# Kernel tuning notes

Measured on AMD Instinct MI355X. Metric: run time of the kernel, lower is better.

## Reference

```python
import jax, jax.numpy as jnp
import numpy as np

B, S, D, H = 4, 2048, 1024, 16
HD = D // H
ROPE_THETA = 10000.0


def setup_inputs() -> dict:
    key = jax.random.key(0)
    ks = jax.random.split(key, 5)
    scale = 1.0 / np.sqrt(D)
    inp = {
        "x": jax.random.normal(ks[0], (B, S, D), dtype=jnp.float32),
        "Wq": jax.random.normal(ks[1], (D, D), dtype=jnp.float32) * scale,
        "bq": jnp.zeros((D,), jnp.float32),
        "Wk": jax.random.normal(ks[2], (D, D), dtype=jnp.float32) * scale,
        "bk": jnp.zeros((D,), jnp.float32),
        "Wv": jax.random.normal(ks[3], (D, D), dtype=jnp.float32) * scale,
        "bv": jnp.zeros((D,), jnp.float32),
        "Wo": jax.random.normal(ks[4], (D, D), dtype=jnp.float32) * scale,
        "bo": jnp.zeros((D,), jnp.float32),
        # causal mask: True means masked (j > i), matching masked_fill semantics
        "attn_mask": jnp.triu(jnp.ones((S, S), dtype=bool), k=1),
    }
    return inp


def _rope(x):
    # x: [B, H, S, HD]; half-split rotary embedding
    half = HD // 2
    inv_freq = 1.0 / (ROPE_THETA ** (jnp.arange(0, half, dtype=jnp.float32) / half))
    pos = jnp.arange(x.shape[2], dtype=jnp.float32)
    freqs = pos[:, None] * inv_freq[None, :]            # [S, half]
    cos = jnp.cos(freqs)[None, None]                    # [1,1,S,half]
    sin = jnp.sin(freqs)[None, None]
    x1, x2 = x[..., :half], x[..., half:]
    return jnp.concatenate([x1 * cos - x2 * sin, x2 * cos + x1 * sin], axis=-1)


def reference(x, Wq, bq, Wk, bk, Wv, bv, Wo, bo, attn_mask):
    def shape(t):  # [B,S,D] -> [B,H,S,HD]
        return t.reshape(B, S, H, HD).transpose(0, 2, 1, 3)

    q = shape(x @ Wq.T + bq)
    k = shape(x @ Wk.T + bk)
    v = shape(x @ Wv.T + bv)
    q = _rope(q)
    k = _rope(k)
    scores = jnp.einsum("bhqd,bhkd->bhqk", q, k) * (HD ** -0.5)
    scores = jnp.where(attn_mask[None, None], -jnp.inf, scores)
    w = jax.nn.softmax(scores, axis=-1)
    attn = jnp.einsum("bhqk,bhkd->bhqd", w, v)
    merged = attn.transpose(0, 2, 1, 3).reshape(B, S, D)
    return merged @ Wo.T + bo
```

## Files before the change

kernel.cpp:

```cpp
#include <hip/hip_runtime.h>
#include <math.h>

#define BATCH 4
#define SEQ   2048
#define DMODEL 1024
#define NHEAD 16
#define HDIM  64
#define MROWS (BATCH*SEQ)

typedef unsigned short u16;
typedef unsigned int   u32;

using bf16x8 = __attribute__((ext_vector_type(8))) short;
using f32x4  = __attribute__((ext_vector_type(4))) float;
using f32x16 = __attribute__((ext_vector_type(16))) float;
using u32x4  = __attribute__((ext_vector_type(4))) unsigned int;

__device__ __forceinline__ u16 f2bf(float f) {
    u32 u = __float_as_uint(f);
    u += 0x7fffu + ((u >> 16) & 1u);
    return (u16)(u >> 16);
}
__device__ __forceinline__ u32 pack2bf(float a, float b) {
    u32 ua = __float_as_uint(a); ua += 0x7fffu + ((ua >> 16) & 1u);
    u32 ub = __float_as_uint(b); ub += 0x7fffu + ((ub >> 16) & 1u);
    return (ua >> 16) | (ub & 0xffff0000u);
}
__device__ __forceinline__ u32 cvtpk(float a, float b) {
    u32 r;
    asm("v_cvt_pk_bf16_f32 %0, %1, %2" : "=v"(r) : "v"(a), "v"(b));
    return r;
}
#define PLSWAP(a, b) asm("v_permlane32_swap_b32 %0, %1" : "+v"(a), "+v"(b))

#define GLOBAL_LOAD_LDS16(gp, lp)                                              \
    __builtin_amdgcn_global_load_lds(                                          \
        (const __attribute__((address_space(1))) void*)(gp),                   \
        (__attribute__((address_space(3))) void*)(lp), 16, 0, 0)

__global__ __launch_bounds__(256) void convert_inputs(
    const float* __restrict__ x,  const float* __restrict__ wq,
    const float* __restrict__ wk, const float* __restrict__ wv,
    const float* __restrict__ wo, u16* __restrict__ dst)
{
    long long i4 = ((long long)blockIdx.x * 256 + threadIdx.x) * 4;
    const float* src; long long off;
    if (i4 < 8388608LL) { src = x; off = i4; }
    else {
        long long j = i4 - 8388608LL;
        int seg = (int)(j >> 20);
        off = j & 1048575LL;
        src = (seg == 0) ? wq : (seg == 1) ? wk : (seg == 2) ? wv : wo;
    }
    float4 v = *(const float4*)(src + off);
    u32 lo = (u32)f2bf(v.x) | ((u32)f2bf(v.y) << 16);
    u32 hi = (u32)f2bf(v.z) | ((u32)f2bf(v.w) << 16);
    *(uint2*)(dst + i4) = make_uint2(lo, hi);
}

template<int QKV>
__global__ __launch_bounds__(512) void gemm_mfma(
    const u16* __restrict__ A,
    const u16* __restrict__ Wq_, const u16* __restrict__ Wk_, const u16* __restrict__ Wv_,
    const float* __restrict__ bq_, const float* __restrict__ bk_, const float* __restrict__ bv_,
    u16* __restrict__ Cq_, u16* __restrict__ Ck_, u16* __restrict__ Cv_,
    float* __restrict__ Cf)
{
    __shared__ u16 As[3 * 256 * 64];
    __shared__ u16 Ws[3 * 128 * 64];

    const int t    = threadIdx.x;
    const int lane = t & 63;
    const int w    = t >> 6;
    const int quad = lane >> 4;
    const int l15  = lane & 15;
    const int wm   = w >> 1;
    const int wn   = w & 1;

    const int bx  = blockIdx.x;
    const int xcd = bx & 7;
    const int i_  = bx >> 3;
    const int bml = i_ & 3;
    const int n_  = i_ >> 2;
    const int seg = (QKV ? (n_ >> 3) : 0);
    const int nn  = (QKV ? (n_ & 7) : n_);

    const u16*   W    = (seg == 0) ? Wq_ : (seg == 1) ? Wk_ : Wv_;
    const float* bias = (seg == 0) ? bq_ : (seg == 1) ? bk_ : bv_;
    u16*         Cb   = (seg == 0) ? Cq_ : (seg == 1) ? Ck_ : Cv_;

    const int bm   = (xcd * 4 + bml) * 256;
    const int bn   = nn * 128;
    const int wrow = wm * 64;
    const int wcol = wn * 64;

    const int sr8 = lane >> 3;
    const int scl = (lane & 7) ^ sr8;
    const u16* gA = A + (size_t)(bm + 8 * w + sr8) * DMODEL + scl * 8;
    const u16* gB = W + (size_t)(bn + 8 * w + sr8) * DMODEL + scl * 8;

#define STAGE_A(li, kt, bs)                                                    \
    GLOBAL_LOAD_LDS16(gA + (size_t)(li) * 64 * DMODEL + (kt) * 64,             \
                      &As[(bs) * 16384 + ((li) * 64 + 8 * w) * 64])
#define STAGE_B(li, kt, bs)                                                    \
    GLOBAL_LOAD_LDS16(gB + (size_t)(li) * 64 * DMODEL + (kt) * 64,             \
                      &Ws[(bs) * 8192 + ((li) * 64 + 8 * w) * 64])

    STAGE_A(0, 0, 0); STAGE_A(1, 0, 0); STAGE_A(2, 0, 0); STAGE_A(3, 0, 0);
    STAGE_B(0, 0, 0); STAGE_B(1, 0, 0);
    STAGE_A(0, 1, 1); STAGE_A(1, 1, 1); STAGE_A(2, 1, 1); STAGE_A(3, 1, 1);
    STAGE_B(0, 1, 1); STAGE_B(1, 1, 1);
    asm volatile("s_waitcnt vmcnt(6)" ::: "memory");
    __builtin_amdgcn_s_barrier();

    const int c0 = (quad ^ (l15 & 7)) * 8;
    const int c1 = c0 ^ 32;

    f32x4 acc[4][4] = {};

    int bsel = 0;
    for (int kt = 0; kt < DMODEL / 64; ++kt) {
        const u16* Ab = &As[bsel * 16384];
        const u16* Bb = &Ws[bsel * 8192];
        const int  ks = kt + 2;
        const int  sb = (bsel >= 1) ? bsel - 1 : 2;
        const bool st = (ks < DMODEL / 64);

        bf16x8 af[4], bf[4];

        #pragma unroll
        for (int i = 0; i < 4; ++i)
            af[i] = *(const bf16x8*)&Ab[(wrow + 16 * i + l15) * 64 + c0];
        #pragma unroll
        for (int j = 0; j < 4; ++j)
            bf[j] = *(const bf16x8*)&Bb[(wcol + 16 * j + l15) * 64 + c0];
        if (st) { STAGE_A(0, ks, sb); STAGE_A(1, ks, sb); STAGE_A(2, ks, sb); }
        __builtin_amdgcn_s_barrier();
        __builtin_amdgcn_s_setprio(1);
        #pragma unroll
        for (int i = 0; i < 4; ++i)
            #pragma unroll
            for (int j = 0; j < 4; ++j)
                acc[i][j] = __builtin_amdgcn_mfma_f32_16x16x32_bf16(af[i], bf[j], acc[i][j], 0, 0, 0);
        __builtin_amdgcn_s_setprio(0);
        __builtin_amdgcn_s_barrier();

        #pragma unroll
        for (int i = 0; i < 4; ++i)
            af[i] = *(const bf16x8*)&Ab[(wrow + 16 * i + l15) * 64 + c1];
        #pragma unroll
        for (int j = 0; j < 4; ++j)
            bf[j] = *(const bf16x8*)&Bb[(wcol + 16 * j + l15) * 64 + c1];
        if (st) { STAGE_A(3, ks, sb); STAGE_B(0, ks, sb); STAGE_B(1, ks, sb); }
        __builtin_amdgcn_s_barrier();
        __builtin_amdgcn_s_setprio(1);
        #pragma unroll
        for (int i = 0; i < 4; ++i)
            #pragma unroll
            for (int j = 0; j < 4; ++j)
                acc[i][j] = __builtin_amdgcn_mfma_f32_16x16x32_bf16(af[i], bf[j], acc[i][j], 0, 0, 0);
        __builtin_amdgcn_s_setprio(0);
        if (st) asm volatile("s_waitcnt vmcnt(6)" ::: "memory");
        else    asm volatile("s_waitcnt vmcnt(0)" ::: "memory");
        __builtin_amdgcn_s_barrier();

        bsel = (bsel == 2) ? 0 : bsel + 1;
    }
#undef STAGE_A
#undef STAGE_B

    float bv[4];
    #pragma unroll
    for (int j = 0; j < 4; j++) bv[j] = bias[bn + wcol + 16 * j + l15];

    if constexpr (QKV == 0) {
        #pragma unroll
        for (int i = 0; i < 4; i++)
            #pragma unroll
            for (int r = 0; r < 4; r++) {
                int mg = bm + wrow + 16 * i + quad * 4 + r;
                #pragma unroll
                for (int j = 0; j < 4; j++)
                    Cf[(size_t)mg * DMODEL + bn + wcol + 16 * j + l15] = acc[i][j][r] + bv[j];
            }
    } else {
        if (seg == 2) {
            u16* T = As;
            #pragma unroll
            for (int i = 0; i < 4; i++) {
                #pragma unroll
                for (int j = 0; j < 4; j++) {
                    int col = wrow + 16 * i + quad * 4;
                    int row = wcol + 16 * j + l15;
                    u32 lo = pack2bf(acc[i][j][0] + bv[j], acc[i][j][1] + bv[j]);
                    u32 hi = pack2bf(acc[i][j][2] + bv[j], acc[i][j][3] + bv[j]);
                    *(uint2*)((char*)T + row * 512 + ((col * 2) ^ ((row & 3) << 4)))
                        = make_uint2(lo, hi);
                }
            }
            __syncthreads();
            {
                int row  = t >> 2, colc = t & 3;
                int hgl  = (bn + row) >> 6;
                int dl   = (bn + row) & 63;
                int bb   = bm >> 11;
                size_t obase = (((size_t)(bb * NHEAD + hgl)) * HDIM + dl) * SEQ
                             + (bm & (SEQ - 1)) + colc * 64;
                #pragma unroll
                for (int k = 0; k < 8; k++) {
                    uint4 vv = *(const uint4*)((const char*)T + row * 512
                                 + ((colc * 128 + k * 16) ^ ((row & 3) << 4)));
                    *(uint4*)(Cb + obase + k * 8) = vv;
                }
            }
        } else {
            const float qscale = (seg == 0) ? 0.18033688011112042f : 1.0f;
            float inv[2];
            #pragma unroll
            for (int j = 0; j < 2; j++) {
                int d = 16 * j + l15;
                inv[j] = exp2f(-(float)d * 0.4152410118609203f);
            }
            #pragma unroll
            for (int i = 0; i < 4; i++)
                #pragma unroll
                for (int r = 0; r < 4; r++) {
                    int mg = bm + wrow + 16 * i + quad * 4 + r;
                    int s  = mg & (SEQ - 1);
                    #pragma unroll
                    for (int j = 0; j < 2; j++) {
                        float f = (float)s * inv[j];
                        float sn, cs;
                        __sincosf(f, &sn, &cs);
                        float a1 = acc[i][j][r]     + bv[j];
                        float a2 = acc[i][j + 2][r] + bv[j + 2];
                        float o1 = (a1 * cs - a2 * sn) * qscale;
                        float o2 = (a2 * cs + a1 * sn) * qscale;
                        Cb[(size_t)mg * DMODEL + bn + wcol + 16 * j       + l15] = f2bf(o1);
                        Cb[(size_t)mg * DMODEL + bn + wcol + 16 * (j + 2) + l15] = f2bf(o2);
                    }
                }
        }
    }
}

__global__ __launch_bounds__(256) void attn_mfma(
    const u16* __restrict__ Q, const u16* __restrict__ K,
    const u16* __restrict__ VT, u16* __restrict__ O)
{
    __shared__ __align__(16) u16 smem[16640];
    u16* const Qs  = smem;
    u16* const Ks0 = smem + 8192;
    u16* const Ks1 = smem;
    u16* const Vt0 = smem + 12288;
    u16* const Vt1 = smem + 4096;
    float* const lS = (float*)(smem + 16384);

    const int t    = threadIdx.x;
    const int lane = t & 63;
    const int w    = t >> 6;
    const int l31  = lane & 31;
    const int hl   = lane >> 5;
    const int bid  = blockIdx.x;
    const int bh   = bid & 63;
    const int x_   = bid >> 6, g_ = x_ >> 2, r_ = x_ & 3;
    const int qt   = (g_ == 0) ? 15 - r_ : (g_ == 1) ? 8 + r_
                   : (g_ == 2) ? 4 + r_ : 3 - r_;
    const int h    = bh & (NHEAD - 1);
    const int b    = bh >> 4;
    const int q0   = qt * 128;

    const size_t gbase = ((size_t)b * SEQ) * DMODEL + h * HDIM;
    const size_t vbase = ((size_t)(b * NHEAD + h)) * HDIM * SEQ;

    const int rl  = lane >> 3;
    const int csw = (lane & 7) ^ rl;

    #pragma unroll
    for (int i = 0; i < 4; i++) {
        int row = 32 * w + 8 * i + rl;
        GLOBAL_LOAD_LDS16(Q + gbase + (size_t)(q0 + row) * DMODEL + csw * 8,
                          &Qs[(32 * w + 8 * i) * 64]);
    }
    #pragma unroll
    for (int i = 0; i < 2; i++) {
        int row = 16 * w + 8 * i + rl;
        GLOBAL_LOAD_LDS16(K + gbase + (size_t)row * DMODEL + csw * 8,
                          &Ks0[(16 * w + 8 * i) * 64]);
        GLOBAL_LOAD_LDS16(VT + vbase + (size_t)row * SEQ + csw * 8,
                          &Vt0[(16 * w + 8 * i) * 64]);
    }
    __syncthreads();

    bf16x8 qf[4];
    {
        int row = 32 * w + l31;
        #pragma unroll
        for (int s = 0; s < 4; s++) {
            int c = (hl + 2 * s) ^ (row & 7);
            qf[s] = *(const bf16x8*)&Qs[row * 64 + c * 8];
        }
    }
    __syncthreads();

    float lsum = 0.0f;
    f32x16 oacc[2] = {};
    const int qg   = q0 + 32 * w + l31;
    const int qmax = q0 + 32 * w + 31;

#define QUADRANT(KRH, F0, F1) do {                                             \
    f32x16 s_ = {};                                                            \
    __builtin_amdgcn_s_setprio(1);                                             \
    _Pragma("unroll")                                                          \
    for (int stp_ = 0; stp_ < 4; ++stp_) {                                     \
        int c_ = ((hl + 2 * stp_) ^ (l31 & 7)) * 8;                            \
        bf16x8 ka_ = *(const bf16x8*)&Ksb[(32 * (KRH) + l31) * 64 + c_];       \
        s_ = __builtin_amdgcn_mfma_f32_32x32x16_bf16(ka_, qf[stp_], s_, 0, 0, 0);\
    }                                                                          \
    __builtin_amdgcn_s_setprio(0);                                             \
    if (k0 + 32 * (KRH) + 31 > q0 + 32 * w) {                                  \
        _Pragma("unroll")                                                      \
        for (int rr_ = 0; rr_ < 16; ++rr_) {                                   \
            int krg_ = k0 + 32 * (KRH) + (rr_ & 3) + 8 * (rr_ >> 2) + 4 * hl;  \
            if (krg_ > qg) s_[rr_] = -1e30f;                                   \
        }                                                                      \
    }                                                                          \
    float pv_[16];                                                             \
    _Pragma("unroll")                                                          \
    for (int rr_ = 0; rr_ < 16; ++rr_) pv_[rr_] = __builtin_amdgcn_exp2f(s_[rr_]);\
    lsum += ((pv_[0]+pv_[1])+(pv_[2]+pv_[3])) + ((pv_[4]+pv_[5])+(pv_[6]+pv_[7]))\
          + ((pv_[8]+pv_[9])+(pv_[10]+pv_[11])) + ((pv_[12]+pv_[13])+(pv_[14]+pv_[15]));\
    u32 k01_ = cvtpk(pv_[0], pv_[1]),   k23_ = cvtpk(pv_[2], pv_[3]);          \
    u32 k45_ = cvtpk(pv_[4], pv_[5]),   k67_ = cvtpk(pv_[6], pv_[7]);          \
    u32 k89_ = cvtpk(pv_[8], pv_[9]),   kab_ = cvtpk(pv_[10], pv_[11]);        \
    u32 kcd_ = cvtpk(pv_[12], pv_[13]), kef_ = cvtpk(pv_[14], pv_[15]);        \
    PLSWAP(k01_, k45_); PLSWAP(k23_, k67_);                                    \
    PLSWAP(k89_, kcd_); PLSWAP(kab_, kef_);                                    \
    { union { u32x4 u; bf16x8 v; } c0_; c0_.u = (u32x4){k01_, k23_, k45_, k67_};\
      F0 = c0_.v; }                                                            \
    { union { u32x4 u; bf16x8 v; } c1_; c1_.u = (u32x4){k89_, kab_, kcd_, kef_};\
      F1 = c1_.v; }                                                            \
} while (0)

#define PVSTEP(STP, PF) do {                                                   \
    int c_ = ((hl + 2 * (STP)) ^ (l31 & 7)) * 8;                               \
    bf16x8 v0_ = *(const bf16x8*)&Vtb[l31 * 64 + c_];                          \
    bf16x8 v1_ = *(const bf16x8*)&Vtb[(32 + l31) * 64 + c_];                   \
    oacc[0] = __builtin_amdgcn_mfma_f32_32x32x16_bf16(PF, v0_, oacc[0], 0, 0, 0);\
    oacc[1] = __builtin_amdgcn_mfma_f32_32x32x16_bf16(PF, v1_, oacc[1], 0, 0, 0);\
} while (0)

    const int ktn = 2 * qt + 2;
    for (int kt = 0; kt < ktn; kt++) {
        const int k0 = kt * 64;
        u16* const Ksb = (kt & 1) ? Ks1 : Ks0;
        u16* const Vtb = (kt & 1) ? Vt1 : Vt0;

        if (kt + 1 < ktn) {
            u16* const Ksn = (kt & 1) ? Ks0 : Ks1;
            u16* const Vtn = (kt & 1) ? Vt0 : Vt1;
            const size_t kk0 = (size_t)(kt + 1) * 64;
            #pragma unroll
            for (int i = 0; i < 2; i++) {
                int row = 16 * w + 8 * i + rl;
                GLOBAL_LOAD_LDS16(K + gbase + (kk0 + row) * DMODEL + csw * 8,
                                  &Ksn[(16 * w + 8 * i) * 64]);
                GLOBAL_LOAD_LDS16(VT + vbase + (size_t)row * SEQ + kk0 + csw * 8,
                                  &Vtn[(16 * w + 8 * i) * 64]);
            }
        }

        if (k0 <= qmax) {
            const bool q2 = (k0 + 32 <= qmax);
            bf16x8 pa0, pa1, pa2, pa3;
            QUADRANT(0, pa0, pa1);
            __builtin_amdgcn_s_setprio(1);
            PVSTEP(0, pa0); PVSTEP(1, pa1);
            __builtin_amdgcn_s_setprio(0);
            if (q2) {
                QUADRANT(1, pa2, pa3);
                __builtin_amdgcn_s_setprio(1);
                PVSTEP(2, pa2); PVSTEP(3, pa3);
                __builtin_amdgcn_s_setprio(0);
            }
        }
        asm volatile("s_waitcnt vmcnt(0)" ::: "memory");
        __builtin_amdgcn_s_barrier();
    }
#undef QUADRANT
#undef PVSTEP

    lsum += __shfl_xor(lsum, 32, 64);
    if (lane < 32) lS[32 * w + lane] = lsum;
    __syncthreads();

    #pragma unroll
    for (int g = 0; g < 4; g++) {
        f32x4 lv = *(const f32x4*)&lS[32 * w + 8 * g + 4 * hl];
        #pragma unroll
        for (int rr = 0; rr < 4; rr++) {
            int qg2 = q0 + 32 * w + rr + 8 * g + 4 * hl;
            float inv = 1.0f / lv[rr];
            #pragma unroll
            for (int dh = 0; dh < 2; dh++) {
                float o = oacc[dh][4 * g + rr] * inv;
                O[gbase + (size_t)qg2 * DMODEL + 32 * dh + l31] = f2bf(o);
            }
        }
    }
}

extern "C" void kernel_launch(void* const* d_in, const int* in_sizes, int n_in,
                              void* d_out, int out_size, void* d_ws, size_t ws_size,
                              hipStream_t stream)
{
    const float* x  = (const float*)d_in[0];
    const float* Wq = (const float*)d_in[1];
    const float* bq = (const float*)d_in[2];
    const float* Wk = (const float*)d_in[3];
    const float* bk = (const float*)d_in[4];
    const float* Wv = (const float*)d_in[5];
    const float* bv = (const float*)d_in[6];
    const float* Wo = (const float*)d_in[7];
    const float* bo = (const float*)d_in[8];

    u16* wsp = (u16*)d_ws;
    u16* xb  = wsp;
    u16* Wqb = wsp + 8388608;
    u16* Wkb = Wqb + 1048576;
    u16* Wvb = Wkb + 1048576;
    u16* Wob = Wvb + 1048576;
    u16* Qb  = Wob + 1048576;
    u16* Kb  = Qb + 8388608;
    u16* Vb  = Kb + 8388608;
    u16* Ab  = Vb + 8388608;

    convert_inputs<<<12288, 256, 0, stream>>>(x, Wq, Wk, Wv, Wo, xb);

    gemm_mfma<1><<<768, 512, 0, stream>>>(xb, Wqb, Wkb, Wvb, bq, bk, bv,
                                          Qb, Kb, Vb, nullptr);

    attn_mfma<<<1024, 256, 0, stream>>>(Qb, Kb, Vb, Ab);

    gemm_mfma<0><<<256, 512, 0, stream>>>(Ab, Wob, nullptr, nullptr, bo, nullptr, nullptr,
                                          nullptr, nullptr, nullptr, (float*)d_out);
}
```

Before: 254.6 us.

## Enlarge GEMM tile to 256x256 with double-buffered 8-phase pipelined K loop

The QKV and output-projection GEMMs move from 256x128 block tiles with a triple-buffered LDS pipeline to 256x256 tiles. Each wave now computes 128x64, with B fragments kept in registers across four sub-phases and loads of the next K tile interleaved between phases. Grid sizes are halved to 384 and 128 blocks. The aim is more arithmetic intensity per LDS and global byte. The costs are more accumulator registers (128 fp32), fewer blocks than the GPU has CUs for the output projection, and a larger LDS swizzle for the V transpose.

```diff
diff --git a/kernel.cpp b/kernel.cpp
--- a/kernel.cpp
+++ b/kernel.cpp
@@ -66,150 +66,162 @@
     u16* __restrict__ Cq_, u16* __restrict__ Ck_, u16* __restrict__ Cv_,
     float* __restrict__ Cf)
 {
-    __shared__ u16 As[3 * 256 * 64];
-    __shared__ u16 Ws[3 * 128 * 64];
+    __shared__ __align__(16) u16 smem[65536];
 
     const int t    = threadIdx.x;
     const int lane = t & 63;
     const int w    = t >> 6;
     const int quad = lane >> 4;
     const int l15  = lane & 15;
-    const int wm   = w >> 1;
-    const int wn   = w & 1;
+    const int wm   = w >> 2;
+    const int wn   = w & 3;
 
     const int bx  = blockIdx.x;
     const int xcd = bx & 7;
     const int i_  = bx >> 3;
     const int bml = i_ & 3;
     const int n_  = i_ >> 2;
-    const int seg = (QKV ? (n_ >> 3) : 0);
-    const int nn  = (QKV ? (n_ & 7) : n_);
+    const int seg = (QKV ? (n_ >> 2) : 0);
+    const int nn  = (QKV ? (n_ & 3) : n_);
 
     const u16*   W    = (seg == 0) ? Wq_ : (seg == 1) ? Wk_ : Wv_;
     const float* bias = (seg == 0) ? bq_ : (seg == 1) ? bk_ : bv_;
     u16*         Cb   = (seg == 0) ? Cq_ : (seg == 1) ? Ck_ : Cv_;
 
-    const int bm   = (xcd * 4 + bml) * 256;
-    const int bn   = nn * 128;
-    const int wrow = wm * 64;
-    const int wcol = wn * 64;
+    const int bm = (xcd * 4 + bml) * 256;
+    const int bn = nn * 256;
 
     const int sr8 = lane >> 3;
     const int scl = (lane & 7) ^ sr8;
     const u16* gA = A + (size_t)(bm + 8 * w + sr8) * DMODEL + scl * 8;
     const u16* gB = W + (size_t)(bn + 8 * w + sr8) * DMODEL + scl * 8;
 
-#define STAGE_A(li, kt, bs)                                                    \
-    GLOBAL_LOAD_LDS16(gA + (size_t)(li) * 64 * DMODEL + (kt) * 64,             \
-                      &As[(bs) * 16384 + ((li) * 64 + 8 * w) * 64])
-#define STAGE_B(li, kt, bs)                                                    \
-    GLOBAL_LOAD_LDS16(gB + (size_t)(li) * 64 * DMODEL + (kt) * 64,             \
-                      &Ws[(bs) * 8192 + ((li) * 64 + 8 * w) * 64])
-
-    STAGE_A(0, 0, 0); STAGE_A(1, 0, 0); STAGE_A(2, 0, 0); STAGE_A(3, 0, 0);
-    STAGE_B(0, 0, 0); STAGE_B(1, 0, 0);
-    STAGE_A(0, 1, 1); STAGE_A(1, 1, 1); STAGE_A(2, 1, 1); STAGE_A(3, 1, 1);
-    STAGE_B(0, 1, 1); STAGE_B(1, 1, 1);
+#define STG_A(rg, kt, bs)                                                      \
+    GLOBAL_LOAD_LDS16(gA + (size_t)(rg) * 64 * DMODEL + (kt) * 64,             \
+                      &smem[(bs) * 16384 + ((rg) * 64 + 8 * w) * 64])
+#define STG_B(rg, kt, bs)                                                      \
+    GLOBAL_LOAD_LDS16(gB + (size_t)(rg) * 64 * DMODEL + (kt) * 64,             \
+                      &smem[32768 + (bs) * 16384 + ((rg) * 64 + 8 * w) * 64])
+
+    STG_B(0, 0, 0); STG_B(1, 0, 0); STG_B(2, 0, 0); STG_B(3, 0, 0);
+    STG_A(0, 0, 0); STG_A(2, 0, 0); STG_A(1, 0, 0); STG_A(3, 0, 0);
+    STG_B(0, 1, 1); STG_B(1, 1, 1); STG_B(2, 1, 1); STG_B(3, 1, 1);
+    STG_A(0, 1, 1); STG_A(2, 1, 1);
     asm volatile("s_waitcnt vmcnt(6)" ::: "memory");
     __builtin_amdgcn_s_barrier();
 
-    const int c0 = (quad ^ (l15 & 7)) * 8;
-    const int c1 = c0 ^ 32;
-
-    f32x4 acc[4][4] = {};
-
-    int bsel = 0;
-    for (int kt = 0; kt < DMODEL / 64; ++kt) {
-        const u16* Ab = &As[bsel * 16384];
-        const u16* Bb = &Ws[bsel * 8192];
-        const int  ks = kt + 2;
-        const int  sb = (bsel >= 1) ? bsel - 1 : 2;
-        const bool st = (ks < DMODEL / 64);
-
-        bf16x8 af[4], bf[4];
-
-        #pragma unroll
-        for (int i = 0; i < 4; ++i)
-            af[i] = *(const bf16x8*)&Ab[(wrow + 16 * i + l15) * 64 + c0];
-        #pragma unroll
-        for (int j = 0; j < 4; ++j)
-            bf[j] = *(const bf16x8*)&Bb[(wcol + 16 * j + l15) * 64 + c0];
-        if (st) { STAGE_A(0, ks, sb); STAGE_A(1, ks, sb); STAGE_A(2, ks, sb); }
-        __builtin_amdgcn_s_barrier();
-        __builtin_amdgcn_s_setprio(1);
-        #pragma unroll
-        for (int i = 0; i < 4; ++i)
-            #pragma unroll
-            for (int j = 0; j < 4; ++j)
-                acc[i][j] = __builtin_amdgcn_mfma_f32_16x16x32_bf16(af[i], bf[j], acc[i][j], 0, 0, 0);
-        __builtin_amdgcn_s_setprio(0);
-        __builtin_amdgcn_s_barrier();
-
-        #pragma unroll
-        for (int i = 0; i < 4; ++i)
-            af[i] = *(const bf16x8*)&Ab[(wrow + 16 * i + l15) * 64 + c1];
-        #pragma unroll
-        for (int j = 0; j < 4; ++j)
-            bf[j] = *(const bf16x8*)&Bb[(wcol + 16 * j + l15) * 64 + c1];
-        if (st) { STAGE_A(3, ks, sb); STAGE_B(0, ks, sb); STAGE_B(1, ks, sb); }
-        __builtin_amdgcn_s_barrier();
-        __builtin_amdgcn_s_setprio(1);
-        #pragma unroll
-        for (int i = 0; i < 4; ++i)
-            #pragma unroll
-            for (int j = 0; j < 4; ++j)
-                acc[i][j] = __builtin_amdgcn_mfma_f32_16x16x32_bf16(af[i], bf[j], acc[i][j], 0, 0, 0);
-        __builtin_amdgcn_s_setprio(0);
-        if (st) asm volatile("s_waitcnt vmcnt(6)" ::: "memory");
-        else    asm volatile("s_waitcnt vmcnt(0)" ::: "memory");
-        __builtin_amdgcn_s_barrier();
-
-        bsel = (bsel == 2) ? 0 : bsel + 1;
-    }
-#undef STAGE_A
-#undef STAGE_B
-
-    float bv[4];
+    const int cA0 = (quad ^ (l15 & 7)) * 8;
+
+    f32x4 acc[8][4] = {};
+    bf16x8 bfr[4][2];
+
+#define LOAD_B(Bb) {                                                           \
+    _Pragma("unroll")                                                          \
+    for (int j = 0; j < 4; ++j) {                                              \
+        bfr[j][0] = *(const bf16x8*)&(Bb)[(wn * 64 + 16 * j + l15) * 64 + cA0];\
+        bfr[j][1] = *(const bf16x8*)&(Bb)[(wn * 64 + 16 * j + l15) * 64 + (cA0 ^ 32)];\
+    } }
+#define PHASE(q, Ab, Bb, STAGES, CKPT) {                                       \
+    bf16x8 af_[2][2];                                                          \
+    if ((q) == 0) LOAD_B(Bb);                                                  \
+    _Pragma("unroll")                                                          \
+    for (int ii = 0; ii < 2; ++ii) {                                           \
+        const int r_ = (wm * 128 + (q) * 32 + 16 * ii + l15) * 64;             \
+        af_[ii][0] = *(const bf16x8*)&(Ab)[r_ + cA0];                          \
+        af_[ii][1] = *(const bf16x8*)&(Ab)[r_ + (cA0 ^ 32)];                   \
+    }                                                                          \
+    STAGES;                                                                    \
+    __builtin_amdgcn_s_barrier();                                              \
+    asm volatile("s_waitcnt lgkmcnt(0)" ::: "memory");                         \
+    __builtin_amdgcn_sched_barrier(0);                                         \
+    __builtin_amdgcn_s_setprio(1);                                             \
+    _Pragma("unroll")                                                          \
+    for (int ii = 0; ii < 2; ++ii)                                             \
+        _Pragma("unroll")                                                      \
+        for (int j = 0; j < 4; ++j) {                                          \
+            acc[2*(q)+ii][j] = __builtin_amdgcn_mfma_f32_16x16x32_bf16(        \
+                af_[ii][0], bfr[j][0], acc[2*(q)+ii][j], 0, 0, 0);             \
+            acc[2*(q)+ii][j] = __builtin_amdgcn_mfma_f32_16x16x32_bf16(        \
+                af_[ii][1], bfr[j][1], acc[2*(q)+ii][j], 0, 0, 0);             \
+        }                                                                      \
+    __builtin_amdgcn_s_setprio(0);                                             \
+    CKPT;                                                                      \
+    __builtin_amdgcn_s_barrier();                                              \
+}
+
+    #pragma unroll 1
+    for (int i = 0; i < 8; ++i) {
+        const bool st = (i < 7);
+        const int  kn = 2 * i + 2, kn3 = 2 * i + 3, ko = 2 * i + 1;
+        {
+            const u16* Ab = smem;
+            const u16* Bb = smem + 32768;
+            PHASE(0, Ab, Bb, { STG_A(1, ko, 1); STG_A(3, ko, 1); }, {});
+            PHASE(1, Ab, Bb, { if (st) { STG_B(0, kn, 0); STG_B(1, kn, 0); } }, {});
+            PHASE(2, Ab, Bb, { if (st) { STG_B(2, kn, 0); STG_B(3, kn, 0); } }, {});
+            PHASE(3, Ab, Bb, { if (st) { STG_A(0, kn, 0); STG_A(2, kn, 0); } },
+                  { if (st) asm volatile("s_waitcnt vmcnt(6)" ::: "memory");
+                    else    asm volatile("s_waitcnt vmcnt(0)" ::: "memory"); });
+        }
+        {
+            const u16* Ab = smem + 16384;
+            const u16* Bb = smem + 32768 + 16384;
+            PHASE(0, Ab, Bb, { if (st) { STG_A(1, kn, 0); STG_A(3, kn, 0); } }, {});
+            PHASE(1, Ab, Bb, { if (st) { STG_B(0, kn3, 1); STG_B(1, kn3, 1); } }, {});
+            PHASE(2, Ab, Bb, { if (st) { STG_B(2, kn3, 1); STG_B(3, kn3, 1); } }, {});
+            PHASE(3, Ab, Bb, { if (st) { STG_A(0, kn3, 1); STG_A(2, kn3, 1); } },
+                  { if (st) asm volatile("s_waitcnt vmcnt(6)" ::: "memory");
+                    else    asm volatile("s_waitcnt vmcnt(0)" ::: "memory"); });
+        }
+    }
+#undef PHASE
+#undef LOAD_B
+#undef STG_A
+#undef STG_B
+
+    const int wrow = wm * 128;
+    const int wcol = wn * 64;
+    float bvv[4];
     #pragma unroll
-    for (int j = 0; j < 4; j++) bv[j] = bias[bn + wcol + 16 * j + l15];
+    for (int j = 0; j < 4; j++) bvv[j] = bias[bn + wcol + 16 * j + l15];
 
     if constexpr (QKV == 0) {
         #pragma unroll
-        for (int i = 0; i < 4; i++)
+        for (int ri = 0; ri < 8; ri++)
             #pragma unroll
             for (int r = 0; r < 4; r++) {
-                int mg = bm + wrow + 16 * i + quad * 4 + r;
+                int mg = bm + wrow + 16 * ri + quad * 4 + r;
                 #pragma unroll
                 for (int j = 0; j < 4; j++)
-                    Cf[(size_t)mg * DMODEL + bn + wcol + 16 * j + l15] = acc[i][j][r] + bv[j];
+                    Cf[(size_t)mg * DMODEL + bn + wcol + 16 * j + l15] = acc[ri][j][r] + bvv[j];
             }
     } else {
         if (seg == 2) {
-            u16* T = As;
-            #pragma unroll
-            for (int i = 0; i < 4; i++) {
+            u16* T = smem;
+            #pragma unroll
+            for (int ri = 0; ri < 8; ri++) {
                 #pragma unroll
                 for (int j = 0; j < 4; j++) {
-                    int col = wrow + 16 * i + quad * 4;
+                    int col = wrow + 16 * ri + quad * 4;
                     int row = wcol + 16 * j + l15;
-                    u32 lo = pack2bf(acc[i][j][0] + bv[j], acc[i][j][1] + bv[j]);
-                    u32 hi = pack2bf(acc[i][j][2] + bv[j], acc[i][j][3] + bv[j]);
-                    *(uint2*)((char*)T + row * 512 + ((col * 2) ^ ((row & 3) << 4)))
+                    u32 lo = pack2bf(acc[ri][j][0] + bvv[j], acc[ri][j][1] + bvv[j]);
+                    u32 hi = pack2bf(acc[ri][j][2] + bvv[j], acc[ri][j][3] + bvv[j]);
+                    *(uint2*)((char*)T + row * 512 + ((col * 2) ^ ((row & 7) << 4)))
                         = make_uint2(lo, hi);
                 }
             }
             __syncthreads();
             {
-                int row  = t >> 2, colc = t & 3;
-                int hgl  = (bn + row) >> 6;
-                int dl   = (bn + row) & 63;
-                int bb   = bm >> 11;
+                int row = t >> 1, half = t & 1;
+                int hgl = (bn + row) >> 6;
+                int dl  = (bn + row) & 63;
+                int bb  = bm >> 11;
                 size_t obase = (((size_t)(bb * NHEAD + hgl)) * HDIM + dl) * SEQ
-                             + (bm & (SEQ - 1)) + colc * 64;
+                             + (bm & (SEQ - 1)) + half * 128;
                 #pragma unroll
-                for (int k = 0; k < 8; k++) {
+                for (int k = 0; k < 16; k++) {
                     uint4 vv = *(const uint4*)((const char*)T + row * 512
-                                 + ((colc * 128 + k * 16) ^ ((row & 3) << 4)));
+                                 + ((half * 256 + k * 16) ^ ((row & 7) << 4)));
                     *(uint4*)(Cb + obase + k * 8) = vv;
                 }
             }
@@ -222,18 +234,18 @@
                 inv[j] = exp2f(-(float)d * 0.4152410118609203f);
             }
             #pragma unroll
-            for (int i = 0; i < 4; i++)
+            for (int ri = 0; ri < 8; ri++)
                 #pragma unroll
                 for (int r = 0; r < 4; r++) {
-                    int mg = bm + wrow + 16 * i + quad * 4 + r;
+                    int mg = bm + wrow + 16 * ri + quad * 4 + r;
                     int s  = mg & (SEQ - 1);
                     #pragma unroll
                     for (int j = 0; j < 2; j++) {
                         float f = (float)s * inv[j];
                         float sn, cs;
                         __sincosf(f, &sn, &cs);
-                        float a1 = acc[i][j][r]     + bv[j];
-                        float a2 = acc[i][j + 2][r] + bv[j + 2];
+                        float a1 = acc[ri][j][r]     + bvv[j];
+                        float a2 = acc[ri][j + 2][r] + bvv[j + 2];
                         float o1 = (a1 * cs - a2 * sn) * qscale;
                         float o2 = (a2 * cs + a1 * sn) * qscale;
                         Cb[(size_t)mg * DMODEL + bn + wcol + 16 * j       + l15] = f2bf(o1);
@@ -437,11 +449,11 @@
 
     convert_inputs<<<12288, 256, 0, stream>>>(x, Wq, Wk, Wv, Wo, xb);
 
-    gemm_mfma<1><<<768, 512, 0, stream>>>(xb, Wqb, Wkb, Wvb, bq, bk, bv,
+    gemm_mfma<1><<<384, 512, 0, stream>>>(xb, Wqb, Wkb, Wvb, bq, bk, bv,
                                           Qb, Kb, Vb, nullptr);
 
     attn_mfma<<<1024, 256, 0, stream>>>(Qb, Kb, Vb, Ab);
 
-    gemm_mfma<0><<<256, 512, 0, stream>>>(Ab, Wob, nullptr, nullptr, bo, nullptr, nullptr,
+    gemm_mfma<0><<<128, 512, 0, stream>>>(Ab, Wob, nullptr, nullptr, bo, nullptr, nullptr,
                                           nullptr, nullptr, nullptr, (float*)d_out);
 }
```

Measured after the change: 265.4 us. 4.2% more time.
